# Kernel optimization log

Measured on AMD Instinct MI355X. Metric: run time of the kernel, lower is better.

Reference implementation:

```python
import jax, jax.numpy as jnp
import numpy as np

IN_F = 256
OUT_F = 256
H = 4
DH = OUT_F // H  # 64
N = 6144


def setup_inputs() -> dict:
    key = jax.random.key(0)
    ks = jax.random.split(key, 6)
    x = jax.random.normal(ks[0], (N, IN_F), dtype=jnp.float32)
    adj = jax.random.randint(ks[1], (N, N), 0, 2, dtype=jnp.int32)
    # per-head Linear(in_features, d_head): weights [H, IN_F, DH], bias [H, DH]
    W = jax.random.normal(ks[2], (H, IN_F, DH), dtype=jnp.float32) / np.sqrt(IN_F)
    Wb = jax.random.normal(ks[3], (H, DH), dtype=jnp.float32) * 0.01
    # per-head Linear(2*d_head, 1): weights [H, 2*DH], bias [H]
    A = jax.random.normal(ks[4], (H, 2 * DH), dtype=jnp.float32) / np.sqrt(2 * DH)
    Ab = jax.random.normal(ks[5], (H,), dtype=jnp.float32) * 0.01
    return {"x": x, "adj": adj, "W": W, "Wb": Wb, "A": A, "Ab": Ab}


def reference(x, adj, W, Wb, A, Ab):
    # h[h,n,d] = per-head linear projection of node features
    h = jnp.einsum("ni,hid->hnd", x, W) + Wb[:, None, :]
    a_src, a_dst = A[:, :DH], A[:, DH:]
    # score(i,j) = a_src . h_i + a_dst . h_j + b  (decomposed concat-linear)
    s_src = jnp.einsum("hnd,hd->hn", h, a_src) + Ab[:, None]  # [H, N]
    s_dst = jnp.einsum("hnd,hd->hn", h, a_dst)                # [H, N]
    scores = s_src[:, :, None] + s_dst[:, None, :]            # [H, N, N]
    # Faithful to source: non-edges get score 0.0 (not -inf) before softmax
    scores = jnp.where(adj[None, :, :] > 0, scores, 0.0)
    probs = jax.nn.softmax(scores, axis=-1)                   # row softmax
    out = jnp.einsum("hij,hjd->hid", probs, h)                # [H, N, DH]
    # concat heads along feature dim -> [N, H*DH]
    return jnp.transpose(out, (1, 0, 2)).reshape(N, H * DH)
```

## Files before the change

### kernel.cpp

```cpp
#include <hip/hip_runtime.h>
#include <stdint.h>

#define NN 6144
#define NC 576

typedef float f32x4 __attribute__((ext_vector_type(4)));
typedef __bf16 bf16x8v __attribute__((ext_vector_type(8)));

__device__ __forceinline__ unsigned short f2bf(float f) {
  unsigned u = __float_as_uint(f);
  u += 0x7FFFu + ((u >> 16) & 1u);
  return (unsigned short)(u >> 16);
}

__device__ __forceinline__ unsigned char f2e4m3(float f) {
  unsigned u = __float_as_uint(f);
  unsigned sgn = (u >> 24) & 0x80u;
  unsigned au = u & 0x7FFFFFFFu;
  if (au >= 0x43E00000u) return (unsigned char)(sgn | 0x7E);
  if (au < 0x3C800000u) {
    int q = (int)rintf(__uint_as_float(au) * 512.0f);
    return (unsigned char)(sgn | (q >= 8 ? 0x08 : q));
  }
  unsigned r = au + 0x7FFFFu + ((au >> 20) & 1u);
  int e = (int)(r >> 23) - 127;
  unsigned m = (r >> 20) & 7u;
  return (unsigned char)(sgn | ((unsigned)(e + 7) << 3) | m);
}

__device__ __forceinline__ unsigned short pack2(float a, float b) {
  return (unsigned short)f2e4m3(a) | ((unsigned short)f2e4m3(b) << 8);
}

__device__ __forceinline__ void async_load16(const void* g, void* l) {
  __builtin_amdgcn_global_load_lds(
      (__attribute__((address_space(1))) void*)(uintptr_t)g,
      (__attribute__((address_space(3))) void*)(uint32_t)(uintptr_t)l,
      16, 0, 0);
}

__global__ __launch_bounds__(256) void p0(
    const int* __restrict__ adj, const float* __restrict__ x,
    const float* __restrict__ W, const float* __restrict__ Aw,
    const float* __restrict__ Wb,
    unsigned char* __restrict__ A8, unsigned short* __restrict__ xsw,
    unsigned short* __restrict__ wsw, float* __restrict__ Acat,
    float* __restrict__ T)
{
  const int bid = blockIdx.x, t = threadIdx.x;
  if (bid < 8) {
#pragma unroll
    for (int i = 0; i < 4; ++i) {
      const int e = bid * 256 + t + i * 2048;
      const int l = e & 63, kc = (e >> 6) & 7, ct = e >> 9;
      const int c = ct * 16 + (l & 15);
      const int h = c >> 6, d = c & 63;
      const int ks = kc * 32 + (l >> 4) * 8;
      const float* src = W + h * 16384 + ks * 64 + d;
      unsigned uu[4];
#pragma unroll
      for (int j = 0; j < 4; ++j)
        uu[j] = (unsigned)f2bf(src[(2*j) * 64]) | ((unsigned)f2bf(src[(2*j+1) * 64]) << 16);
      *(uint4*)(wsw + (size_t)e * 8) = (uint4){uu[0], uu[1], uu[2], uu[3]};
    }
    return;
  }
  if (bid == 8) {
    T[t] = 0.f;
    const int h = t >> 6, d = t & 63;
    Acat[t]       = Aw[h * 128 + d];
    Acat[256 + t] = Aw[h * 128 + 64 + d];
    Acat[512 + t] = Wb[t];
    return;
  }
  if (bid < 33) {
    const int tid = (bid - 9) * 256 + t;
#pragma unroll 4
    for (int i = 0; i < 32; ++i) {
      const int e = tid + i * 6144;
      const int l = e & 63, kc = (e >> 6) & 7, mt = e >> 9;
      const int node = mt * 16 + (l & 15);
      const int ks = kc * 32 + (l >> 4) * 8;
      const float4* xp = (const float4*)(x + (size_t)node * 256 + ks);
      float4 v0 = xp[0], v1 = xp[1];
      uint4 o;
      o.x = (unsigned)f2bf(v0.x) | ((unsigned)f2bf(v0.y) << 16);
      o.y = (unsigned)f2bf(v0.z) | ((unsigned)f2bf(v0.w) << 16);
      o.z = (unsigned)f2bf(v1.x) | ((unsigned)f2bf(v1.y) << 16);
      o.w = (unsigned)f2bf(v1.z) | ((unsigned)f2bf(v1.w) << 16);
      *(uint4*)(xsw + (size_t)e * 8) = o;
    }
    return;
  }
  const int pb = bid - 33;
  const int4* a4 = (const int4*)adj;
  unsigned* o1 = (unsigned*)A8;
  const int g0 = pb * 2048 + t;
  int4 q[8];
#pragma unroll
  for (int j = 0; j < 8; ++j) q[j] = a4[g0 + j * 256];
#pragma unroll
  for (int j = 0; j < 8; ++j)
    o1[g0 + j * 256] = (unsigned)q[j].x * 0x38u | (unsigned)q[j].y * 0x3800u |
                       (unsigned)q[j].z * 0x380000u | (unsigned)q[j].w * 0x38000000u;
}

__global__ __launch_bounds__(256) void k1_mfma(
    const unsigned short* __restrict__ xsw, const unsigned short* __restrict__ wsw,
    const float* __restrict__ Acat, const float* __restrict__ Ab,
    unsigned char* __restrict__ V8, float* __restrict__ e_src, float* __restrict__ T)
{
  __shared__ unsigned char lv[4][4096];
  __shared__ float lt[256];
  const int t = threadIdx.x;
  const int w = t >> 6, l = t & 63;
  const int v = blockIdx.x * 4 + w;
  const int mt = v >> 1, nh = v & 1;
  const int i0 = mt * 16, c0 = nh * 128;
  const int lm = l & 15, lk = l >> 4;

  lt[t] = 0.f;
  __syncthreads();

  f32x4 acc[8];
#pragma unroll
  for (int nt = 0; nt < 8; ++nt) acc[nt] = (f32x4){0.f, 0.f, 0.f, 0.f};

  const unsigned short* ap = xsw + ((size_t)mt * 512 + l) * 8;
  const unsigned short* bp = wsw + ((size_t)nh * 4096 + l) * 8;

#pragma unroll
  for (int kc = 0; kc < 8; ++kc) {
    bf16x8v a = *(const bf16x8v*)(ap + (size_t)kc * 512);
#pragma unroll
    for (int nt = 0; nt < 8; ++nt) {
      bf16x8v b = *(const bf16x8v*)(bp + ((size_t)nt * 512 + kc * 64) * 8);
      acc[nt] = __builtin_amdgcn_mfma_f32_16x16x32_bf16(a, b, acc[nt], 0, 0, 0);
    }
  }

  float asv[8], adv[8];
#pragma unroll
  for (int nt = 0; nt < 8; ++nt) {
    const int cc = c0 + nt * 16 + lm;
    const float wb = Acat[512 + cc];
#pragma unroll
    for (int rr = 0; rr < 4; ++rr) acc[nt][rr] += wb;
    asv[nt] = Acat[cc];
    adv[nt] = Acat[256 + cc];
  }

#pragma unroll
  for (int nt = 0; nt < 8; ++nt)
    atomicAdd(&lt[c0 + nt * 16 + lm], acc[nt][0] + acc[nt][1] + acc[nt][2] + acc[nt][3]);

  float ss[2][4], sd[2][4];
#pragma unroll
  for (int hl = 0; hl < 2; ++hl)
#pragma unroll
    for (int rr = 0; rr < 4; ++rr) {
      float s1 = 0.f, s2 = 0.f;
#pragma unroll
      for (int j = 0; j < 4; ++j) {
        s1 += acc[hl * 4 + j][rr] * asv[hl * 4 + j];
        s2 += acc[hl * 4 + j][rr] * adv[hl * 4 + j];
      }
      ss[hl][rr] = s1; sd[hl][rr] = s2;
    }
#pragma unroll
  for (int off = 1; off < 16; off <<= 1)
#pragma unroll
    for (int hl = 0; hl < 2; ++hl)
#pragma unroll
      for (int rr = 0; rr < 4; ++rr) {
        ss[hl][rr] += __shfl_xor(ss[hl][rr], off);
        sd[hl][rr] += __shfl_xor(sd[hl][rr], off);
      }

  float ed[2][4];
#pragma unroll
  for (int hl = 0; hl < 2; ++hl)
#pragma unroll
    for (int rr = 0; rr < 4; ++rr) ed[hl][rr] = expf(sd[hl][rr]);

  if (lm == 0) {
#pragma unroll
    for (int hl = 0; hl < 2; ++hl) {
      const int hh = nh * 2 + hl;
      const float ab = Ab[hh];
#pragma unroll
      for (int rr = 0; rr < 4; ++rr)
        e_src[(size_t)hh * NN + i0 + lk * 4 + rr] = expf(ss[hl][rr] + ab);
    }
  }

  unsigned char* mylv = lv[w];
#pragma unroll
  for (int nt = 0; nt < 8; ++nt) {
    const int hl = nt >> 2;
    const int d = (nt & 3) * 16 + lm;
    const int lcE = hl * 128 + d;
    const int lcP = lcE + 64;
    *(unsigned short*)(mylv + lcE * 16 + lk * 4)     = pack2(ed[hl][0] * acc[nt][0], ed[hl][1] * acc[nt][1]);
    *(unsigned short*)(mylv + lcE * 16 + lk * 4 + 2) = pack2(ed[hl][2] * acc[nt][2], ed[hl][3] * acc[nt][3]);
    *(unsigned short*)(mylv + lcP * 16 + lk * 4)     = pack2(acc[nt][0], acc[nt][1]);
    *(unsigned short*)(mylv + lcP * 16 + lk * 4 + 2) = pack2(acc[nt][2], acc[nt][3]);
  }
#pragma unroll
  for (int j = 0; j < 4; ++j) {
    const int lc = j * 64 + l;
    uint4 val = *(const uint4*)(mylv + lc * 16);
    *(uint4*)(V8 + (size_t)(nh * 256 + lc) * NN + i0) = val;
  }
  if (lm == 0) {
#pragma unroll
    for (int hl = 0; hl < 2; ++hl) {
      const int hh = nh * 2 + hl;
      unsigned char* pq = V8 + (size_t)(512 + hh) * NN + i0 + lk * 4;
      *(unsigned short*)pq       = pack2(ed[hl][0], ed[hl][1]);
      *(unsigned short*)(pq + 2) = pack2(ed[hl][2], ed[hl][3]);
    }
    if (nh == 0)
      *(unsigned*)(V8 + (size_t)516 * NN + i0 + lk * 4) = 0x38383838u;
  }

  __syncthreads();
  atomicAdd(&T[t], lt[t]);
}

__global__ __launch_bounds__(256, 3) void k2_gemm(
    const unsigned char* __restrict__ A8, const unsigned char* __restrict__ V8,
    float* __restrict__ out2, int nks)
{
  __shared__ unsigned char lB[144 * 64];
  const int t   = threadIdx.x;
  const int bid = blockIdx.x;
  const int cb  = bid & 3;
  const int rb  = (bid >> 2) & 31;
  const int ks  = bid >> 7;
  const int krange = NN / nks;
  const int i0 = rb * 192, n0 = cb * 144, k0 = ks * krange;
  const int w = t >> 6, l = t & 63;
  const int lm = l & 15, lk = l >> 4;

  f32x4 acc[3][9];
#pragma unroll
  for (int mt = 0; mt < 3; ++mt)
#pragma unroll
    for (int nt = 0; nt < 9; ++nt) acc[mt][nt] = (f32x4){0.f, 0.f, 0.f, 0.f};

  const unsigned char* gA0 = A8 + (size_t)(i0 + w * 48 + lm) * NN + k0 + lk * 16;

  const int iters = krange / 64;
  for (int it = 0; it < iters; ++it) {
    const int kb = k0 + it * 64;
    {
      const unsigned char* gB = V8 + (size_t)n0 * NN + kb;
#pragma unroll
      for (int u = 0; u < 2; ++u) {
        const int gi = u * 256 + t;
        const int col = gi >> 2;
        const int g = (gi & 3) ^ ((col ^ (col >> 2)) & 3);
        async_load16(gB + (size_t)col * NN + g * 16,
                     (char*)lB + (size_t)(u * 256 + (t & ~63)) * 16);
      }
      if (t < 64) {
        const int gi = 512 + t;
        const int col = gi >> 2;
        const int g = (gi & 3) ^ ((col ^ (col >> 2)) & 3);
        async_load16(gB + (size_t)col * NN + g * 16, (char*)lB + (size_t)512 * 16);
      }
    }
    longlong2 afr[3];
    const unsigned char* gA = gA0 + it * 64;
#pragma unroll
    for (int mt = 0; mt < 3; ++mt)
      afr[mt] = *(const longlong2*)(gA + (size_t)mt * 16 * NN);
    __syncthreads();
#pragma unroll
    for (int ks2 = 0; ks2 < 2; ++ks2) {
#pragma unroll
      for (int nt = 0; nt < 9; ++nt) {
        const int cc = nt * 16 + lm;
        const int sc = (cc ^ (cc >> 2)) & 3;
        long b = *(const long*)(lB + cc * 64 + ((lk ^ sc) * 16) + ks2 * 8);
#pragma unroll
        for (int mt = 0; mt < 3; ++mt)
          acc[mt][nt] = __builtin_amdgcn_mfma_f32_16x16x32_fp8_fp8(
              ks2 ? afr[mt].y : afr[mt].x, b, acc[mt][nt], 0, 0, 0);
      }
    }
    __syncthreads();
  }

  float* o = out2 + (size_t)ks * ((size_t)NN * NC);
  const int row0 = i0 + w * 48 + lk * 4;
  const int colb = n0 + lm;
#pragma unroll
  for (int mt = 0; mt < 3; ++mt)
#pragma unroll
    for (int nt = 0; nt < 9; ++nt)
#pragma unroll
      for (int rr = 0; rr < 4; ++rr)
        o[(size_t)(row0 + mt * 16 + rr) * NC + colb + nt * 16] = acc[mt][nt][rr];
}

__global__ __launch_bounds__(256) void k3_final(
    const float* __restrict__ out2, const float* __restrict__ e_src,
    const float* __restrict__ T, float* __restrict__ out, int nks)
{
  const int n = blockIdx.x, c = threadIdx.x;
  const int h = c >> 6, d = c & 63;
  float Se = 0.f, Sp = 0.f, E = 0.f, dg = 0.f;
  for (int s = 0; s < nks; ++s) {
    const float* ra = out2 + (size_t)s * ((size_t)NN * NC) + (size_t)n * NC;
    Se += ra[h * 128 + d];
    Sp += ra[h * 128 + 64 + d];
    E  += ra[512 + h];
    dg += ra[516];
  }
  float e = e_src[h * NN + n];
  float D = e * E + ((float)NN - dg);
  out[(size_t)n * 256 + c] = (e * Se + (T[c] - Sp)) / D;
}

extern "C" void kernel_launch(void* const* d_in, const int* in_sizes, int n_in,
                              void* d_out, int out_size, void* d_ws, size_t ws_size,
                              hipStream_t stream) {
  const float* x  = (const float*)d_in[0];
  const int*   adj= (const int*)d_in[1];
  const float* W  = (const float*)d_in[2];
  const float* Wb = (const float*)d_in[3];
  const float* Aw = (const float*)d_in[4];
  const float* Ab = (const float*)d_in[5];
  float* out = (float*)d_out;
  char* ws = (char*)d_ws;
  unsigned char* V8 = (unsigned char*)ws;
  float* e_src = (float*)(ws + 3538944);
  float* T     = (float*)(ws + 3637248);
  float* Acat  = (float*)(ws + 3638272);
  unsigned short* wsw = (unsigned short*)(ws + 3641344);
  unsigned short* xsw = (unsigned short*)(ws + 3772416);
  unsigned char* A8   = (unsigned char*)(ws + 6918144);
  float* out2  = (float*)(ws + 44666880);

  const size_t slab = (size_t)NN * NC * 4;
  const size_t base = 44666880;
  int nks = 2;
  if (ws_size >= base + 6 * slab)      nks = 6;
  else if (ws_size >= base + 4 * slab) nks = 4;

  hipLaunchKernelGGL(p0, dim3(4641), dim3(256), 0, stream,
                     adj, x, W, Aw, Wb, A8, xsw, wsw, Acat, T);
  hipLaunchKernelGGL(k1_mfma, dim3(192), dim3(256), 0, stream,
                     xsw, wsw, Acat, Ab, V8, e_src, T);
  hipLaunchKernelGGL(k2_gemm, dim3(128 * nks), dim3(256), 0, stream, A8, V8, out2, nks);
  hipLaunchKernelGGL(k3_final, dim3(NN), dim3(256), 0, stream, out2, e_src, T, out, nks);
}
```

Measured before the change: 319.0 us.

## Double-buffer LDS B tiles and prefetch A fragments in the fp8 GEMM

The k2_gemm main loop now uses two LDS buffers for the B tile. It issues the async global-to-LDS loads for the next k-block, plus the register loads of the next A fragments, before running the MFMAs on the current buffer. This lets memory latency overlap with compute and drops one __syncthreads per iteration. In exchange, LDS use per block doubles and register pressure rises for the prefetched A fragments, which could affect occupancy under the 3-blocks-per-CU launch bound.

After: 337.4 us. +5.8%, slower.

```diff
diff --git a/kernel.cpp b/kernel.cpp
--- a/kernel.cpp
+++ b/kernel.cpp
@@ -232,7 +232,7 @@
     const unsigned char* __restrict__ A8, const unsigned char* __restrict__ V8,
     float* __restrict__ out2, int nks)
 {
-  __shared__ unsigned char lB[144 * 64];
+  __shared__ unsigned char lB[2][144 * 64];
   const int t   = threadIdx.x;
   const int bid = blockIdx.x;
   const int cb  = bid & 3;
@@ -243,6 +243,12 @@
   const int w = t >> 6, l = t & 63;
   const int lm = l & 15, lk = l >> 4;
 
+  const int gi0  = t,       col0 = gi0 >> 2,  g0s = (gi0 & 3) ^ ((col0 ^ (col0 >> 2)) & 3);
+  const int gi1  = 256 + t, col1 = gi1 >> 2,  g1s = (gi1 & 3) ^ ((col1 ^ (col1 >> 2)) & 3);
+  const int gi2  = 512 + t, col2 = gi2 >> 2,  g2s = (gi2 & 3) ^ ((col2 ^ (col2 >> 2)) & 3);
+  const int d0s = (t & ~63) * 16;
+  const int d1s = (256 + (t & ~63)) * 16;
+
   f32x4 acc[3][9];
 #pragma unroll
   for (int mt = 0; mt < 3; ++mt)
@@ -250,47 +256,58 @@
     for (int nt = 0; nt < 9; ++nt) acc[mt][nt] = (f32x4){0.f, 0.f, 0.f, 0.f};
 
   const unsigned char* gA0 = A8 + (size_t)(i0 + w * 48 + lm) * NN + k0 + lk * 16;
+  const unsigned char* gBb = V8 + (size_t)n0 * NN;
 
   const int iters = krange / 64;
+
+  {
+    const unsigned char* gB = gBb + k0;
+    async_load16(gB + (size_t)col0 * NN + g0s * 16, (char*)lB[0] + d0s);
+    async_load16(gB + (size_t)col1 * NN + g1s * 16, (char*)lB[0] + d1s);
+    if (t < 64)
+      async_load16(gB + (size_t)col2 * NN + g2s * 16, (char*)lB[0] + 512 * 16);
+  }
+  longlong2 afr[3];
+#pragma unroll
+  for (int mt = 0; mt < 3; ++mt)
+    afr[mt] = *(const longlong2*)(gA0 + (size_t)mt * 16 * NN);
+
+  int p = 0;
   for (int it = 0; it < iters; ++it) {
-    const int kb = k0 + it * 64;
-    {
-      const unsigned char* gB = V8 + (size_t)n0 * NN + kb;
-#pragma unroll
-      for (int u = 0; u < 2; ++u) {
-        const int gi = u * 256 + t;
-        const int col = gi >> 2;
-        const int g = (gi & 3) ^ ((col ^ (col >> 2)) & 3);
-        async_load16(gB + (size_t)col * NN + g * 16,
-                     (char*)lB + (size_t)(u * 256 + (t & ~63)) * 16);
-      }
-      if (t < 64) {
-        const int gi = 512 + t;
-        const int col = gi >> 2;
-        const int g = (gi & 3) ^ ((col ^ (col >> 2)) & 3);
-        async_load16(gB + (size_t)col * NN + g * 16, (char*)lB + (size_t)512 * 16);
-      }
-    }
-    longlong2 afr[3];
-    const unsigned char* gA = gA0 + it * 64;
-#pragma unroll
-    for (int mt = 0; mt < 3; ++mt)
-      afr[mt] = *(const longlong2*)(gA + (size_t)mt * 16 * NN);
     __syncthreads();
+    longlong2 nxt[3];
+    if (it + 1 < iters) {
+      const int kb1 = k0 + (it + 1) * 64;
+      const unsigned char* gB = gBb + kb1;
+      unsigned char* dst = lB[1 - p];
+      async_load16(gB + (size_t)col0 * NN + g0s * 16, (char*)dst + d0s);
+      async_load16(gB + (size_t)col1 * NN + g1s * 16, (char*)dst + d1s);
+      if (t < 64)
+        async_load16(gB + (size_t)col2 * NN + g2s * 16, (char*)dst + 512 * 16);
+      const unsigned char* gA = gA0 + (it + 1) * 64;
+#pragma unroll
+      for (int mt = 0; mt < 3; ++mt)
+        nxt[mt] = *(const longlong2*)(gA + (size_t)mt * 16 * NN);
+    }
+    const unsigned char* buf = lB[p];
 #pragma unroll
     for (int ks2 = 0; ks2 < 2; ++ks2) {
 #pragma unroll
       for (int nt = 0; nt < 9; ++nt) {
         const int cc = nt * 16 + lm;
         const int sc = (cc ^ (cc >> 2)) & 3;
-        long b = *(const long*)(lB + cc * 64 + ((lk ^ sc) * 16) + ks2 * 8);
+        long b = *(const long*)(buf + cc * 64 + ((lk ^ sc) * 16) + ks2 * 8);
 #pragma unroll
         for (int mt = 0; mt < 3; ++mt)
           acc[mt][nt] = __builtin_amdgcn_mfma_f32_16x16x32_fp8_fp8(
               ks2 ? afr[mt].y : afr[mt].x, b, acc[mt][nt], 0, 0, 0);
       }
     }
-    __syncthreads();
+    if (it + 1 < iters) {
+#pragma unroll
+      for (int mt = 0; mt < 3; ++mt) afr[mt] = nxt[mt];
+    }
+    p ^= 1;
   }
 
   float* o = out2 + (size_t)ks * ((size_t)NN * NC);
```
